# Performance work log

Measured on AMD Instinct MI355X. Metric: run time of the kernel, lower is better.

The kernel has to match this reference:

```python
import jax, jax.numpy as jnp
import numpy as np

N_BLOCK = 3; EMBED = 256; N_HEAD = 8; HEAD = EMBED // N_HEAD
N_AGENT = 8; SEQ = 256; BATCH = 64; ACT_DIM = 32
DECAY_SCALE = 1.0
EPS = 1e-6


def _decay_matrix():
    # Per-head decay kappas as in Mava Sable, decay over timesteps (pos // n_agent), causal mask.
    gammas = (1.0 - jnp.exp(jnp.linspace(jnp.log(1.0 / 32.0), jnp.log(1.0 / 512.0), N_HEAD))) * DECAY_SCALE
    t = (jnp.arange(SEQ) // N_AGENT).astype(jnp.float32)
    diff = t[:, None] - t[None, :]
    causal = jnp.arange(SEQ)[:, None] >= jnp.arange(SEQ)[None, :]
    return jnp.where(causal[None], gammas[:, None, None] ** diff[None], 0.0)  # [H,S,S]


def rmsnorm(x, scale):
    return x * jax.lax.rsqrt(jnp.mean(x * x, -1, keepdims=True) + EPS) * scale


def groupnorm(x, scale, bias):
    # GroupNorm with n_head groups over the feature dim, per position.
    B, S, E = x.shape
    xg = x.reshape(B, S, N_HEAD, HEAD)
    mu = xg.mean(-1, keepdims=True)
    var = ((xg - mu) ** 2).mean(-1, keepdims=True)
    xn = ((xg - mu) * jax.lax.rsqrt(var + 1e-5)).reshape(B, S, E)
    return xn * scale + bias


def retention(q_in, k_in, v_in, wq, wk, wv, wg, wo, gns, gnb, decay):
    # Parallel multi-scale retention: (Q K^T * D) V, groupnorm, swish gate from query input.
    B, S, E = q_in.shape
    q = (q_in @ wq).reshape(B, S, N_HEAD, HEAD).transpose(0, 2, 1, 3)
    k = (k_in @ wk).reshape(B, S, N_HEAD, HEAD).transpose(0, 2, 1, 3) / jnp.sqrt(jnp.float32(HEAD))
    v = (v_in @ wv).reshape(B, S, N_HEAD, HEAD).transpose(0, 2, 1, 3)
    scores = jnp.einsum('bhnd,bhmd->bhnm', q, k) * decay[None]
    ret = jnp.einsum('bhnm,bhmd->bhnd', scores, v)
    ret = groupnorm(ret.transpose(0, 2, 1, 3).reshape(B, S, E), gns, gnb)
    return (jax.nn.swish(q_in @ wg) * ret) @ wo


def swiglu(x, wg, w1, w2):
    return (jax.nn.swish(x @ wg) * (x @ w1)) @ w2


def forward(action, obs_rep, w_enc, ln0, wq1, wk1, wv1, wg1, wo1, gns1, gnb1, ln1,
            wq2, wk2, wv2, wg2, wo2, gns2, gnb2, ln2, swg, sw1, sw2, ln3,
            hw1, hb1, hln, hw2, hb2):
    decay = _decay_matrix()
    x = rmsnorm(jax.nn.gelu(action @ w_enc), ln0)
    for b in range(N_BLOCK):
        r1 = retention(x, x, x, wq1[b], wk1[b], wv1[b], wg1[b], wo1[b], gns1[b], gnb1[b], decay)
        x = rmsnorm(x + r1, ln1[b])
        r2 = retention(obs_rep, x, x, wq2[b], wk2[b], wv2[b], wg2[b], wo2[b], gns2[b], gnb2[b], decay)
        x = rmsnorm(obs_rep + r2, ln2[b])
        x = rmsnorm(x + swiglu(x, swg[b], sw1[b], sw2[b]), ln3[b])
    h = rmsnorm(jax.nn.gelu(x @ hw1 + hb1), hln)
    return h @ hw2 + hb2


def setup_inputs() -> dict:
    key = jax.random.key(0)
    ks = jax.random.split(key, 24)
    E, A, NB = EMBED, ACT_DIM, N_BLOCK
    s = 0.02
    return {
        'action': jax.random.uniform(ks[0], (BATCH, SEQ, A), jnp.float32),
        'obs_rep': jax.random.normal(ks[1], (BATCH, SEQ, E), jnp.float32),
        'w_enc': jax.random.normal(ks[2], (A, E), jnp.float32) * s,
        'ln0': jnp.ones((E,), jnp.float32),
        'wq1': jax.random.normal(ks[3], (NB, E, E), jnp.float32) * s,
        'wk1': jax.random.normal(ks[4], (NB, E, E), jnp.float32) * s,
        'wv1': jax.random.normal(ks[5], (NB, E, E), jnp.float32) * s,
        'wg1': jax.random.normal(ks[6], (NB, E, E), jnp.float32) * s,
        'wo1': jax.random.normal(ks[7], (NB, E, E), jnp.float32) * s,
        'gns1': jnp.ones((NB, E), jnp.float32),
        'gnb1': jnp.zeros((NB, E), jnp.float32),
        'ln1': jnp.ones((NB, E), jnp.float32),
        'wq2': jax.random.normal(ks[8], (NB, E, E), jnp.float32) * s,
        'wk2': jax.random.normal(ks[9], (NB, E, E), jnp.float32) * s,
        'wv2': jax.random.normal(ks[10], (NB, E, E), jnp.float32) * s,
        'wg2': jax.random.normal(ks[11], (NB, E, E), jnp.float32) * s,
        'wo2': jax.random.normal(ks[12], (NB, E, E), jnp.float32) * s,
        'gns2': jnp.ones((NB, E), jnp.float32),
        'gnb2': jnp.zeros((NB, E), jnp.float32),
        'ln2': jnp.ones((NB, E), jnp.float32),
        'swg': jax.random.normal(ks[13], (NB, E, E), jnp.float32) * s,
        'sw1': jax.random.normal(ks[14], (NB, E, E), jnp.float32) * s,
        'sw2': jax.random.normal(ks[15], (NB, E, E), jnp.float32) * s,
        'ln3': jnp.ones((NB, E), jnp.float32),
        'hw1': jax.random.normal(ks[16], (E, E), jnp.float32) * s,
        'hb1': jnp.zeros((E,), jnp.float32),
        'hln': jnp.ones((E,), jnp.float32),
        'hw2': jax.random.normal(ks[17], (E, A), jnp.float32) * s,
        'hb2': jnp.zeros((A,), jnp.float32),
    }


def reference(action, obs_rep, w_enc, ln0, wq1, wk1, wv1, wg1, wo1, gns1, gnb1, ln1,
              wq2, wk2, wv2, wg2, wo2, gns2, gnb2, ln2, swg, sw1, sw2, ln3,
              hw1, hb1, hln, hw2, hb2):
    return forward(action, obs_rep, w_enc, ln0, wq1, wk1, wv1, wg1, wo1, gns1, gnb1, ln1,
                   wq2, wk2, wv2, wg2, wo2, gns2, gnb2, ln2, swg, sw1, sw2, ln3,
                   hw1, hb1, hln, hw2, hb2)
```

## Files before the change

kernel.cpp:

```cpp
#include <hip/hip_runtime.h>
#include <cstdint>
#include <cmath>

typedef __attribute__((ext_vector_type(8))) short short8;
typedef __attribute__((ext_vector_type(4))) float floatx4;

#define DEV static __device__ __forceinline__

DEV float bf2f(uint16_t u) {
    union { uint32_t i; float f; } v; v.i = ((uint32_t)u) << 16; return v.f;
}
DEV uint16_t f2bf(float f) {
    union { float f; uint32_t i; } v; v.f = f;
    uint32_t r = (v.i + 0x7FFFu + ((v.i >> 16) & 1u)) >> 16;
    return (uint16_t)r;
}
DEV float swishf(float x) { return x / (1.f + __expf(-x)); }
DEV float geluf(float x) {
    const float c = 0.7978845608028654f;
    float t = tanhf(c * (x + 0.044715f * x * x * x));
    return 0.5f * x * (1.f + t);
}

#define CHUNK_E 8192
#define MAT_E   65536
#define APAD    264


struct TArg { const float* src[15]; };

__global__ __launch_bounds__(256) void tpose_k(TArg ta, uint16_t* __restrict__ arena) {
    int z = blockIdx.z;
    const float* src; uint16_t* dst;
    if (z == 0) {
        if (blockIdx.y) return;
        src = ta.src[0]; dst = arena;
    } else if (z <= 39) {
        int q = z - 1; int ti = q / 3, s = q % 3;
        src = ta.src[1 + ti] + (size_t)s * 65536;
        dst = arena + CHUNK_E + (size_t)(ti * 3 + s) * MAT_E;
    } else {
        src = ta.src[14]; dst = arena + CHUNK_E + (size_t)39 * MAT_E;
    }
    int k0 = blockIdx.y << 5;
    int n0 = blockIdx.x << 6;
    __shared__ __align__(16) uint16_t tile[32][72];
    int t = threadIdx.x;
    {
        int r = t >> 3, c = (t & 7) << 3;
        const float* s0 = src + (size_t)(k0 + r) * 256 + n0 + c;
        float4 f0 = *(const float4*)s0;
        float4 f1 = *(const float4*)(s0 + 4);
        tile[r][c + 0] = f2bf(f0.x); tile[r][c + 1] = f2bf(f0.y);
        tile[r][c + 2] = f2bf(f0.z); tile[r][c + 3] = f2bf(f0.w);
        tile[r][c + 4] = f2bf(f1.x); tile[r][c + 5] = f2bf(f1.y);
        tile[r][c + 6] = f2bf(f1.z); tile[r][c + 7] = f2bf(f1.w);
    }
    __syncthreads();
    {
        int n = t >> 2, c = (t & 3) << 3;
        uint16_t tmp[8];
#pragma unroll
        for (int j = 0; j < 8; ++j) tmp[j] = tile[c + j][n];
        *(uint4*)&dst[(size_t)(k0 >> 5) * CHUNK_E + (size_t)(n0 + n) * 32 + c] = *(uint4*)tmp;
    }
}

struct SegArgs {
    const float* action; const float* obs;
    uint16_t *actb, *obsb, *xb, *bq, *bk, *bv, *bg, *brg;
    const float *ln0, *hb1, *hln, *hw2, *hb2;
    float* outp;
    float l2g[8];
};

enum { EP2_NONE = 0, EP2_SWIGLU = 1 };

DEV void stage32(const uint16_t* __restrict__ g, int m0, uint16_t* __restrict__ lds) {
    const int t = threadIdx.x;
#pragma unroll
    for (int j = 0; j < 2; ++j) {
        int u = t + (j << 9);
        int r = u >> 5, cc = (u & 31) << 3;
        *(short8*)(lds + (size_t)r * APAD + cc) =
            *(const short8*)(g + (size_t)(m0 + r) * 256 + cc);
    }
}

template<bool AL, bool OG, bool RL, bool GELU>
DEV void gemm_ks(int m0, const uint16_t* __restrict__ A, const uint16_t* __restrict__ Wt,
                 uint16_t* __restrict__ Og, uint16_t* __restrict__ Ol,
                 const float* __restrict__ bias,
                 const uint16_t* __restrict__ Rg, const uint16_t* __restrict__ Rl,
                 const float* __restrict__ lnw,
                 float (&rowsum)[8][32], float (&red)[4][32][64])
{
    const int t = threadIdx.x;
    const int w = t >> 6, lane = t & 63, l16 = lane & 15, lg = lane >> 4;
    const int wc = w & 3, cb = wc << 6;
    const int kbase = (w >> 2) << 2;

    floatx4 acc[2][4];
#pragma unroll
    for (int i = 0; i < 2; ++i)
#pragma unroll
        for (int j = 0; j < 4; ++j) acc[i][j] = (floatx4){0.f, 0.f, 0.f, 0.f};

#pragma unroll
    for (int k2 = 0; k2 < 4; ++k2) {
        const int kc = kbase + k2;
        short8 aF[2], bF[4];
#pragma unroll
        for (int rt = 0; rt < 2; ++rt) {
            int row = (rt << 4) + l16;
            if constexpr (AL)
                aF[rt] = *(const short8*)(A + (size_t)row * APAD + (kc << 5) + (lg << 3));
            else
                aF[rt] = *(const short8*)(A + (size_t)(m0 + row) * 256 + (kc << 5) + (lg << 3));
        }
#pragma unroll
        for (int ct = 0; ct < 4; ++ct)
            bF[ct] = *(const short8*)(Wt + (size_t)kc * CHUNK_E +
                                      (size_t)(cb + (ct << 4) + l16) * 32 + (lg << 3));
#pragma unroll
        for (int rt = 0; rt < 2; ++rt)
#pragma unroll
            for (int ct = 0; ct < 4; ++ct)
                acc[rt][ct] = __builtin_amdgcn_mfma_f32_16x16x32_bf16(
                    aF[rt], bF[ct], acc[rt][ct], 0, 0, 0);
    }

    if (w >= 4) {
#pragma unroll
        for (int rt = 0; rt < 2; ++rt)
#pragma unroll
            for (int ct = 0; ct < 4; ++ct)
#pragma unroll
                for (int r = 0; r < 4; ++r)
                    red[wc][(rt << 4) | (ct << 2) | r][lane] = acc[rt][ct][r];
    }
    __syncthreads();

    float v[2][4][4];
    if (w < 4) {
#pragma unroll
        for (int rt = 0; rt < 2; ++rt)
#pragma unroll
            for (int ct = 0; ct < 4; ++ct)
#pragma unroll
                for (int r = 0; r < 4; ++r) {
                    int row = (rt << 4) + (lg << 2) + r;
                    int col = cb + (ct << 4) + l16;
                    float x = acc[rt][ct][r] + red[wc][(rt << 4) | (ct << 2) | r][lane];
                    if constexpr (GELU) {
                        if (bias) x += bias[col];
                        x = geluf(x);
                    } else {
                        if constexpr (RL) x += bf2f(Rl[(size_t)row * APAD + col]);
                        else              x += bf2f(Rg[(size_t)(m0 + row) * 256 + col]);
                    }
                    v[rt][ct][r] = x;
                }
#pragma unroll
        for (int rt = 0; rt < 2; ++rt)
#pragma unroll
            for (int r = 0; r < 4; ++r) {
                float p = 0.f;
#pragma unroll
                for (int ct = 0; ct < 4; ++ct) p += v[rt][ct][r] * v[rt][ct][r];
                p += __shfl_xor(p, 1, 64); p += __shfl_xor(p, 2, 64);
                p += __shfl_xor(p, 4, 64); p += __shfl_xor(p, 8, 64);
                int row = (rt << 4) + (lg << 2) + r;
                if (l16 == 0) rowsum[w][row] = p;
            }
    }
    __syncthreads();
    if (w < 4) {
#pragma unroll
        for (int rt = 0; rt < 2; ++rt)
#pragma unroll
            for (int r = 0; r < 4; ++r) {
                int row = (rt << 4) + (lg << 2) + r;
                float tot = rowsum[0][row] + rowsum[1][row] + rowsum[2][row] + rowsum[3][row];
                float rn = rsqrtf(tot * (1.f / 256.f) + 1e-6f);
#pragma unroll
                for (int ct = 0; ct < 4; ++ct) {
                    int col = cb + (ct << 4) + l16;
                    uint16_t bb = f2bf(v[rt][ct][r] * rn * lnw[col]);
                    if constexpr (OG)
                        Og[(size_t)(m0 + row) * 256 + col] = bb;
                    Ol[(size_t)row * APAD + col] = bb;
                }
            }
    }
    __syncthreads();
}

template<int EPI, bool AL>
DEV void gemm2_ws(int m0, const uint16_t* __restrict__ A,
                  const uint16_t* __restrict__ W1, const uint16_t* __restrict__ W2,
                  uint16_t* __restrict__ O1, uint16_t* __restrict__ O2,
                  uint16_t* __restrict__ Ol, float (&red)[4][32][64])
{
    const int t = threadIdx.x;
    const int w = t >> 6, lane = t & 63, l16 = lane & 15, lg = lane >> 4;
    const int wc = w & 3, cb = wc << 6;
    const uint16_t* W = (w < 4) ? W1 : W2;

    floatx4 acc[2][4];
#pragma unroll
    for (int i = 0; i < 2; ++i)
#pragma unroll
        for (int j = 0; j < 4; ++j) acc[i][j] = (floatx4){0.f, 0.f, 0.f, 0.f};

#pragma unroll
    for (int kc = 0; kc < 8; ++kc) {
        short8 aF[2], bF[4];
#pragma unroll
        for (int rt = 0; rt < 2; ++rt) {
            int row = (rt << 4) + l16;
            if constexpr (AL)
                aF[rt] = *(const short8*)(A + (size_t)row * APAD + (kc << 5) + (lg << 3));
            else
                aF[rt] = *(const short8*)(A + (size_t)(m0 + row) * 256 + (kc << 5) + (lg << 3));
        }
#pragma unroll
        for (int ct = 0; ct < 4; ++ct)
            bF[ct] = *(const short8*)(W + (size_t)kc * CHUNK_E +
                                      (size_t)(cb + (ct << 4) + l16) * 32 + (lg << 3));
#pragma unroll
        for (int rt = 0; rt < 2; ++rt)
#pragma unroll
            for (int ct = 0; ct < 4; ++ct)
                acc[rt][ct] = __builtin_amdgcn_mfma_f32_16x16x32_bf16(
                    aF[rt], bF[ct], acc[rt][ct], 0, 0, 0);
    }

    if constexpr (EPI == EP2_NONE) {
        uint16_t* O = (w < 4) ? O1 : O2;
#pragma unroll
        for (int rt = 0; rt < 2; ++rt)
#pragma unroll
            for (int ct = 0; ct < 4; ++ct)
#pragma unroll
                for (int r = 0; r < 4; ++r) {
                    int row = (rt << 4) + (lg << 2) + r;
                    int col = cb + (ct << 4) + l16;
                    O[(size_t)(m0 + row) * 256 + col] = f2bf(acc[rt][ct][r]);
                }
    } else {
        if (w >= 4) {
#pragma unroll
            for (int rt = 0; rt < 2; ++rt)
#pragma unroll
                for (int ct = 0; ct < 4; ++ct)
#pragma unroll
                    for (int r = 0; r < 4; ++r)
                        red[wc][(rt << 4) | (ct << 2) | r][lane] = acc[rt][ct][r];
        }
        __syncthreads();
        if (w < 4) {
#pragma unroll
            for (int rt = 0; rt < 2; ++rt)
#pragma unroll
                for (int ct = 0; ct < 4; ++ct)
#pragma unroll
                    for (int r = 0; r < 4; ++r) {
                        int row = (rt << 4) + (lg << 2) + r;
                        int col = cb + (ct << 4) + l16;
                        float up = red[wc][(rt << 4) | (ct << 2) | r][lane];
                        Ol[(size_t)row * APAD + col] = f2bf(swishf(acc[rt][ct][r]) * up);
                    }
        }
    }
}

DEV void gemm_enc(int m0, const uint16_t* __restrict__ A, const uint16_t* __restrict__ Wt,
                  uint16_t* __restrict__ Og, uint16_t* __restrict__ Ol,
                  const float* __restrict__ lnw, float (&rowsum)[8][32])
{
    const int t = threadIdx.x;
    const int w = t >> 6, lane = t & 63, l16 = lane & 15, lg = lane >> 4;

    floatx4 acc[2][2];
#pragma unroll
    for (int i = 0; i < 2; ++i)
#pragma unroll
        for (int j = 0; j < 2; ++j) acc[i][j] = (floatx4){0.f, 0.f, 0.f, 0.f};

    short8 aF[2], bF[2];
#pragma unroll
    for (int rt = 0; rt < 2; ++rt)
        aF[rt] = *(const short8*)(A + (size_t)((rt << 4) + l16) * 40 + (lg << 3));
#pragma unroll
    for (int ct = 0; ct < 2; ++ct)
        bF[ct] = *(const short8*)(Wt + (size_t)((w << 5) + (ct << 4) + l16) * 32 + (lg << 3));
#pragma unroll
    for (int rt = 0; rt < 2; ++rt)
#pragma unroll
        for (int ct = 0; ct < 2; ++ct)
            acc[rt][ct] = __builtin_amdgcn_mfma_f32_16x16x32_bf16(
                aF[rt], bF[ct], acc[rt][ct], 0, 0, 0);

    float v[2][2][4];
#pragma unroll
    for (int rt = 0; rt < 2; ++rt)
#pragma unroll
        for (int ct = 0; ct < 2; ++ct)
#pragma unroll
            for (int r = 0; r < 4; ++r)
                v[rt][ct][r] = geluf(acc[rt][ct][r]);

#pragma unroll
    for (int rt = 0; rt < 2; ++rt)
#pragma unroll
        for (int r = 0; r < 4; ++r) {
            float p = v[rt][0][r] * v[rt][0][r] + v[rt][1][r] * v[rt][1][r];
            p += __shfl_xor(p, 1, 64); p += __shfl_xor(p, 2, 64);
            p += __shfl_xor(p, 4, 64); p += __shfl_xor(p, 8, 64);
            int row = (rt << 4) + (lg << 2) + r;
            if (l16 == 0) rowsum[w][row] = p;
        }
    __syncthreads();
#pragma unroll
    for (int rt = 0; rt < 2; ++rt)
#pragma unroll
        for (int r = 0; r < 4; ++r) {
            int row = (rt << 4) + (lg << 2) + r;
            float tot = rowsum[0][row] + rowsum[1][row] + rowsum[2][row] + rowsum[3][row]
                      + rowsum[4][row] + rowsum[5][row] + rowsum[6][row] + rowsum[7][row];
            float rn = rsqrtf(tot * (1.f / 256.f) + 1e-6f);
#pragma unroll
            for (int ct = 0; ct < 2; ++ct) {
                int col = (w << 5) + (ct << 4) + l16;
                uint16_t bb = f2bf(v[rt][ct][r] * rn * lnw[col]);
                Og[(size_t)(m0 + row) * 256 + col] = bb;
                Ol[(size_t)row * APAD + col] = bb;
            }
        }
    __syncthreads();
}

DEV int rowbase(int blk) { return (blk & 63) * 256 + (blk >> 6) * 32; }


__global__ __launch_bounds__(512, 4) void seg0_k(SegArgs sa, const uint16_t* __restrict__ wenc,
                                                 const uint16_t* __restrict__ wq,
                                                 const uint16_t* __restrict__ wk,
                                                 const uint16_t* __restrict__ wv,
                                                 const uint16_t* __restrict__ wg)
{
    __shared__ float rowsum[8][32];
    __shared__ float red[4][32][64];
    __shared__ __align__(16) uint16_t actS[32][40];
    __shared__ __align__(16) uint16_t T0[32][APAD];
    const int t = threadIdx.x;
    const int m0 = rowbase(blockIdx.x);
    if (t < 256) {
        int r = t >> 3, c = (t & 7) << 2;
        float4 f = *(const float4*)(sa.action + (size_t)(m0 + r) * 32 + c);
        uint16_t tmp[4] = { f2bf(f.x), f2bf(f.y), f2bf(f.z), f2bf(f.w) };
        *(uint2*)&actS[r][c] = *(uint2*)tmp;
    }
    {
        const float4* ob = (const float4*)sa.obs + (size_t)m0 * 64;
        uint2* od = (uint2*)sa.obsb + (size_t)m0 * 64;
#pragma unroll
        for (int j = 0; j < 4; ++j) {
            float4 f = ob[(j << 9) + t];
            uint16_t tmp[4] = { f2bf(f.x), f2bf(f.y), f2bf(f.z), f2bf(f.w) };
            od[(j << 9) + t] = *(uint2*)tmp;
        }
    }
    __syncthreads();
    gemm_enc(m0, &actS[0][0], wenc, sa.xb, &T0[0][0], sa.ln0, rowsum);
    gemm2_ws<EP2_NONE, true>(m0, &T0[0][0], wq, wk, sa.bq, sa.bk, nullptr, red);
    gemm2_ws<EP2_NONE, true>(m0, &T0[0][0], wv, wg, sa.bv, sa.bg, nullptr, red);
}

__global__ __launch_bounds__(512, 4) void attn_k(SegArgs sa, const float* __restrict__ gns,
                                                 const float* __restrict__ gnb)
{
    __shared__ __align__(16) uint16_t QS[256][40];
    __shared__ __align__(16) uint16_t Ks[256][40];
    __shared__ __align__(16) uint16_t Vt[32][264];
    const int b = blockIdx.x & 63, h = blockIdx.x >> 6;
    const float l2g = sa.l2g[h];
    const int t = threadIdx.x, w = t >> 6, lane = t & 63, l16 = lane & 15, lg = lane >> 4;
    const size_t base = ((size_t)b * 256) * 256 + (size_t)h * 32;
    const uint16_t *q = sa.bq, *kbuf = sa.bk, *vbuf = sa.bv, *g = sa.bg;
    uint16_t* out = sa.brg;

    if (t < 256) {
        const uint4* qr = (const uint4*)(q + base + (size_t)t * 256);
        *(uint4*)&QS[t][0] = qr[0]; *(uint4*)&QS[t][8] = qr[1];
        *(uint4*)&QS[t][16] = qr[2]; *(uint4*)&QS[t][24] = qr[3];
        const uint4* kr = (const uint4*)(kbuf + base + (size_t)t * 256);
        *(uint4*)&Ks[t][0] = kr[0]; *(uint4*)&Ks[t][8] = kr[1];
        *(uint4*)&Ks[t][16] = kr[2]; *(uint4*)&Ks[t][24] = kr[3];
    } else {
        int c = t - 256;
        union { uint4 v4[4]; uint16_t u[32]; } vv;
        const uint4* vr = (const uint4*)(vbuf + base + (size_t)c * 256);
        vv.v4[0] = vr[0]; vv.v4[1] = vr[1]; vv.v4[2] = vr[2]; vv.v4[3] = vr[3];
#pragma unroll
        for (int d = 0; d < 32; ++d) Vt[d][c] = vv.u[d];
    }
    __syncthreads();

    const int iA = w, iB = 15 - w;
    short8 qFA = *(const short8*)&QS[(iA << 4) + l16][lg << 3];
    short8 qFB = *(const short8*)&QS[(iB << 4) + l16][lg << 3];

    const float invsq = 0.17677669529663687f;

    floatx4 raccA[2], raccB[2];
    raccA[0] = (floatx4){0,0,0,0}; raccA[1] = (floatx4){0,0,0,0};
    raccB[0] = (floatx4){0,0,0,0}; raccB[1] = (floatx4){0,0,0,0};

    auto do_strip = [&](int si, short8 qF, floatx4 (&racc)[2]) {
        const int jtmax = ((si << 4) + 15) >> 5;
        for (int jt = 0; jt <= jtmax; ++jt) {
            const int j0 = jt << 5;
            floatx4 sacc[2];
            sacc[0] = (floatx4){0,0,0,0}; sacc[1] = (floatx4){0,0,0,0};
            short8 kF[2];
#pragma unroll
            for (int ct = 0; ct < 2; ++ct)
                kF[ct] = *(const short8*)&Ks[j0 + (ct << 4) + l16][lg << 3];
#pragma unroll
            for (int ct = 0; ct < 2; ++ct)
                sacc[ct] = __builtin_amdgcn_mfma_f32_16x16x32_bf16(
                    qF, kF[ct], sacc[ct], 0, 0, 0);
#pragma unroll
            for (int ct = 0; ct < 2; ++ct)
#pragma unroll
                for (int r = 0; r < 4; ++r) {
                    int row16 = (lg << 2) + r;
                    int i = (si << 4) + row16;
                    int j = j0 + (ct << 4) + l16;
                    float svv = 0.f;
                    if (i >= j)
                        svv = sacc[ct][r] * invsq *
                              exp2f((float)((i >> 3) - (j >> 3)) * l2g);
                    QS[(si << 4) + row16][(ct << 4) + l16] = f2bf(svv);
                }
            short8 vF[2];
#pragma unroll
            for (int ct = 0; ct < 2; ++ct)
                vF[ct] = *(const short8*)&Vt[(ct << 4) + l16][j0 + (lg << 3)];
            short8 sF = *(const short8*)&QS[(si << 4) + l16][lg << 3];
#pragma unroll
            for (int ct = 0; ct < 2; ++ct)
                racc[ct] = __builtin_amdgcn_mfma_f32_16x16x32_bf16(
                    sF, vF[ct], racc[ct], 0, 0, 0);
        }
    };
    do_strip(iA, qFA, raccA);
    do_strip(iB, qFB, raccB);

    auto epi = [&](int si, floatx4 (&racc)[2]) {
#pragma unroll
        for (int r = 0; r < 4; ++r) {
            float v0 = racc[0][r], v1 = racc[1][r];
            float s1 = v0 + v1, s2 = v0 * v0 + v1 * v1;
            s1 += __shfl_xor(s1, 1, 64); s2 += __shfl_xor(s2, 1, 64);
            s1 += __shfl_xor(s1, 2, 64); s2 += __shfl_xor(s2, 2, 64);
            s1 += __shfl_xor(s1, 4, 64); s2 += __shfl_xor(s2, 4, 64);
            s1 += __shfl_xor(s1, 8, 64); s2 += __shfl_xor(s2, 8, 64);
            float mu = s1 * (1.f / 32.f);
            float var = s2 * (1.f / 32.f) - mu * mu;
            float rstd = rsqrtf(var + 1e-5f);
            int srow = (si << 4) + (lg << 2) + r;
            size_t obase = ((size_t)b * 256 + srow) * 256 + (size_t)h * 32;
#pragma unroll
            for (int ct = 0; ct < 2; ++ct) {
                int d = (ct << 4) + l16;
                float x = ct ? v1 : v0;
                float y = (x - mu) * rstd * gns[h * 32 + d] + gnb[h * 32 + d];
                float gv = swishf(bf2f(g[obase + d]));
                out[obase + d] = f2bf(y * gv);
            }
        }
    };
    epi(iA, raccA);
    epi(iB, raccB);
}

__global__ __launch_bounds__(512, 4) void g1_k(SegArgs sa,
    const uint16_t* __restrict__ wo, const float* __restrict__ ln1,
    const uint16_t* __restrict__ wq, const uint16_t* __restrict__ wk,
    const uint16_t* __restrict__ wv, const uint16_t* __restrict__ wg)
{
    __shared__ float rowsum[8][32];
    __shared__ float red[4][32][64];
    __shared__ __align__(16) uint16_t T0[32][APAD];
    __shared__ __align__(16) uint16_t T1[32][APAD];
    const int m0 = rowbase(blockIdx.x);
    stage32(sa.brg, m0, &T1[0][0]);
    __syncthreads();
    gemm_ks<true, false, false, false>(m0, &T1[0][0], wo,
        nullptr, &T0[0][0], nullptr, sa.xb, nullptr, ln1, rowsum, red);
    stage32(sa.obsb, m0, &T1[0][0]);
    gemm2_ws<EP2_NONE, true>(m0, &T0[0][0], wk, wv, sa.bk, sa.bv, nullptr, red);
    __syncthreads();
    gemm2_ws<EP2_NONE, true>(m0, &T1[0][0], wq, wg, sa.bq, sa.bg, nullptr, red);
}

__global__ __launch_bounds__(512, 4) void g2_k(SegArgs sa,
    const uint16_t* __restrict__ wo, const float* __restrict__ ln2,
    const uint16_t* __restrict__ wswg, const uint16_t* __restrict__ wsw1,
    const uint16_t* __restrict__ wsw2, const float* __restrict__ ln3,
    const uint16_t* __restrict__ nwq, const uint16_t* __restrict__ nwk,
    const uint16_t* __restrict__ nwv, const uint16_t* __restrict__ nwg)
{
    __shared__ float rowsum[8][32];
    __shared__ float red[4][32][64];
    __shared__ __align__(16) uint16_t T0[32][APAD];
    __shared__ __align__(16) uint16_t T1[32][APAD];
    const int m0 = rowbase(blockIdx.x);
    stage32(sa.brg, m0, &T1[0][0]);
    __syncthreads();
    gemm_ks<true, false, false, false>(m0, &T1[0][0], wo,
        nullptr, &T0[0][0], nullptr, sa.obsb, nullptr, ln2, rowsum, red);
    gemm2_ws<EP2_SWIGLU, true>(m0, &T0[0][0], wswg, wsw1, nullptr, nullptr, &T1[0][0], red);
    __syncthreads();
    gemm_ks<true, true, true, false>(m0, &T1[0][0], wsw2,
        sa.xb, &T0[0][0], nullptr, nullptr, &T0[0][0], ln3, rowsum, red);
    if (nwq) {
        gemm2_ws<EP2_NONE, true>(m0, &T0[0][0], nwq, nwk, sa.bq, sa.bk, nullptr, red);
        gemm2_ws<EP2_NONE, true>(m0, &T0[0][0], nwv, nwg, sa.bv, sa.bg, nullptr, red);
    }
}

__global__ __launch_bounds__(512, 4) void head_k(SegArgs sa, const uint16_t* __restrict__ hw1t)
{
    __shared__ float rowsum[8][32];
    __shared__ float red[4][32][64];
    __shared__ __align__(16) uint16_t T0[32][APAD];
    const int t = threadIdx.x;
    const int m0 = rowbase(blockIdx.x);
    gemm_ks<false, false, false, true>(m0, sa.xb, hw1t,
        nullptr, &T0[0][0], sa.hb1, nullptr, nullptr, sa.hln, rowsum, red);
    float* w2s = &red[0][0][0];
#pragma unroll
    for (int j = 0; j < 16; ++j) w2s[(j << 9) + t] = sa.hw2[(j << 9) + t];
    __syncthreads();
    {
        int n = t & 31, rs = t >> 5;
#pragma unroll
        for (int rr = 0; rr < 2; ++rr) {
            int lrow = (rr << 4) + rs;
            float a0 = sa.hb2[n];
#pragma unroll 8
            for (int kk = 0; kk < 256; ++kk)
                a0 += bf2f(T0[lrow][kk]) * w2s[kk * 32 + n];
            sa.outp[(size_t)(m0 + lrow) * 32 + n] = a0;
        }
    }
}

extern "C" void kernel_launch(void* const* d_in, const int* in_sizes, int n_in,
                              void* d_out, int out_size, void* d_ws, size_t ws_size,
                              hipStream_t stream)
{
    const float* action = (const float*)d_in[0];
    const float* obs    = (const float*)d_in[1];
    const float* w_enc  = (const float*)d_in[2];
    const float* ln0    = (const float*)d_in[3];
    const float* wq1 = (const float*)d_in[4];
    const float* wk1 = (const float*)d_in[5];
    const float* wv1 = (const float*)d_in[6];
    const float* wg1 = (const float*)d_in[7];
    const float* wo1 = (const float*)d_in[8];
    const float* gns1 = (const float*)d_in[9];
    const float* gnb1 = (const float*)d_in[10];
    const float* ln1  = (const float*)d_in[11];
    const float* wq2 = (const float*)d_in[12];
    const float* wk2 = (const float*)d_in[13];
    const float* wv2 = (const float*)d_in[14];
    const float* wg2 = (const float*)d_in[15];
    const float* wo2 = (const float*)d_in[16];
    const float* gns2 = (const float*)d_in[17];
    const float* gnb2 = (const float*)d_in[18];
    const float* ln2  = (const float*)d_in[19];
    const float* swgp = (const float*)d_in[20];
    const float* sw1p = (const float*)d_in[21];
    const float* sw2p = (const float*)d_in[22];
    const float* ln3  = (const float*)d_in[23];
    const float* hw1  = (const float*)d_in[24];
    const float* hb1  = (const float*)d_in[25];
    const float* hln  = (const float*)d_in[26];
    const float* hw2  = (const float*)d_in[27];
    const float* hb2  = (const float*)d_in[28];

    char* ws = (char*)d_ws;
    uint16_t* wt   = (uint16_t*)(ws + 0);
    uint16_t* actb = (uint16_t*)(ws + 6291456);
    uint16_t* obsb = (uint16_t*)(ws + 7340032);
    uint16_t* xb   = (uint16_t*)(ws + 15728640);
    uint16_t* bq   = (uint16_t*)(ws + 24117248);
    uint16_t* bk   = (uint16_t*)(ws + 32505856);
    uint16_t* bv   = (uint16_t*)(ws + 40894464);
    uint16_t* bg   = (uint16_t*)(ws + 49283072);
    uint16_t* brg  = (uint16_t*)(ws + 57671680);

    uint16_t* wtenc = wt;
    uint16_t* hw1t  = wt + CHUNK_E + (size_t)39 * MAT_E;
    auto WTp = [&](int ti, int s) { return wt + CHUNK_E + (size_t)(ti * 3 + s) * MAT_E; };

    TArg ta;
    ta.src[0] = w_enc;
    ta.src[1] = wq1;  ta.src[2] = wk1;  ta.src[3] = wv1;  ta.src[4] = wg1;  ta.src[5] = wo1;
    ta.src[6] = wq2;  ta.src[7] = wk2;  ta.src[8] = wv2;  ta.src[9] = wg2;  ta.src[10] = wo2;
    ta.src[11] = swgp; ta.src[12] = sw1p; ta.src[13] = sw2p; ta.src[14] = hw1;
    tpose_k<<<dim3(4, 8, 41), 256, 0, stream>>>(ta, wt);

    SegArgs sa;
    sa.action = action; sa.obs = obs;
    sa.actb = actb; sa.obsb = obsb; sa.xb = xb;
    sa.bq = bq; sa.bk = bk; sa.bv = bv; sa.bg = bg; sa.brg = brg;
    sa.ln0 = ln0; sa.hb1 = hb1; sa.hln = hln; sa.hw2 = hw2; sa.hb2 = hb2;
    sa.outp = (float*)d_out;
    {
        const double a = log(1.0 / 32.0), bb = log(1.0 / 512.0);
        for (int hh = 0; hh < 8; ++hh) {
            double lg = a + (bb - a) * hh / 7.0;
            double gam = 1.0 - exp(lg);
            sa.l2g[hh] = (float)(log(gam) / log(2.0));
        }
    }

    dim3 GB(512), TB(512);
    seg0_k<<<GB, TB, 0, stream>>>(sa, wtenc, WTp(0, 0), WTp(1, 0), WTp(2, 0), WTp(3, 0));
    for (int b3 = 0; b3 < 3; ++b3) {
        attn_k<<<GB, TB, 0, stream>>>(sa, gns1 + b3 * 256, gnb1 + b3 * 256);
        g1_k<<<GB, TB, 0, stream>>>(sa, WTp(4, b3), ln1 + b3 * 256,
                                    WTp(5, b3), WTp(6, b3), WTp(7, b3), WTp(8, b3));
        attn_k<<<GB, TB, 0, stream>>>(sa, gns2 + b3 * 256, gnb2 + b3 * 256);
        g2_k<<<GB, TB, 0, stream>>>(sa, WTp(9, b3), ln2 + b3 * 256,
                                    WTp(10, b3), WTp(11, b3), WTp(12, b3), ln3 + b3 * 256,
                                    b3 < 2 ? WTp(0, b3 + 1) : nullptr,
                                    b3 < 2 ? WTp(1, b3 + 1) : nullptr,
                                    b3 < 2 ? WTp(2, b3 + 1) : nullptr,
                                    b3 < 2 ? WTp(3, b3 + 1) : nullptr);
    }
    head_k<<<GB, TB, 0, stream>>>(sa, hw1t);
}
```

Measured before the change: 496.1 us.

## Prefetch weight fragments up front and split split-K epilogue across all waves

In the split-K GEMM, all weight fragments for a wave's K half are loaded into registers before the MFMA loop. The reduction is restructured so each K-half wave group finishes one row tile, which spreads the residual/GELU, RMSNorm and store epilogue over all 8 waves instead of 4. In the two-weight GEMM, weight fragments are loaded in a double-buffered prefetch so the second half's loads overlap the first half's MFMAs. The aim is to hide global weight-load latency and remove idle waves in the epilogue, at the cost of more registers (16 short8 fragments per wave), which may reduce occupancy or cause spills.

```diff
diff --git a/kernel.cpp b/kernel.cpp
--- a/kernel.cpp
+++ b/kernel.cpp
@@ -98,7 +98,16 @@
     const int t = threadIdx.x;
     const int w = t >> 6, lane = t & 63, l16 = lane & 15, lg = lane >> 4;
     const int wc = w & 3, cb = wc << 6;
-    const int kbase = (w >> 2) << 2;
+    const int kh = w >> 2;
+    const int kbase = kh << 2;
+
+    short8 bF[4][4];
+#pragma unroll
+    for (int k2 = 0; k2 < 4; ++k2)
+#pragma unroll
+        for (int ct = 0; ct < 4; ++ct)
+            bF[k2][ct] = *(const short8*)(Wt + (size_t)(kbase + k2) * CHUNK_E +
+                                          (size_t)(cb + (ct << 4) + l16) * 32 + (lg << 3));
 
     floatx4 acc[2][4];
 #pragma unroll
@@ -109,7 +118,7 @@
 #pragma unroll
     for (int k2 = 0; k2 < 4; ++k2) {
         const int kc = kbase + k2;
-        short8 aF[2], bF[4];
+        short8 aF[2];
 #pragma unroll
         for (int rt = 0; rt < 2; ++rt) {
             int row = (rt << 4) + l16;
@@ -119,79 +128,85 @@
                 aF[rt] = *(const short8*)(A + (size_t)(m0 + row) * 256 + (kc << 5) + (lg << 3));
         }
 #pragma unroll
-        for (int ct = 0; ct < 4; ++ct)
-            bF[ct] = *(const short8*)(Wt + (size_t)kc * CHUNK_E +
-                                      (size_t)(cb + (ct << 4) + l16) * 32 + (lg << 3));
-#pragma unroll
         for (int rt = 0; rt < 2; ++rt)
 #pragma unroll
             for (int ct = 0; ct < 4; ++ct)
                 acc[rt][ct] = __builtin_amdgcn_mfma_f32_16x16x32_bf16(
-                    aF[rt], bF[ct], acc[rt][ct], 0, 0, 0);
-    }
-
-    if (w >= 4) {
-#pragma unroll
-        for (int rt = 0; rt < 2; ++rt)
-#pragma unroll
-            for (int ct = 0; ct < 4; ++ct)
-#pragma unroll
-                for (int r = 0; r < 4; ++r)
-                    red[wc][(rt << 4) | (ct << 2) | r][lane] = acc[rt][ct][r];
-    }
-    __syncthreads();
-
-    float v[2][4][4];
-    if (w < 4) {
-#pragma unroll
-        for (int rt = 0; rt < 2; ++rt)
-#pragma unroll
-            for (int ct = 0; ct < 4; ++ct)
-#pragma unroll
-                for (int r = 0; r < 4; ++r) {
-                    int row = (rt << 4) + (lg << 2) + r;
-                    int col = cb + (ct << 4) + l16;
-                    float x = acc[rt][ct][r] + red[wc][(rt << 4) | (ct << 2) | r][lane];
-                    if constexpr (GELU) {
-                        if (bias) x += bias[col];
-                        x = geluf(x);
-                    } else {
-                        if constexpr (RL) x += bf2f(Rl[(size_t)row * APAD + col]);
-                        else              x += bf2f(Rg[(size_t)(m0 + row) * 256 + col]);
-                    }
-                    v[rt][ct][r] = x;
-                }
-#pragma unroll
-        for (int rt = 0; rt < 2; ++rt)
-#pragma unroll
-            for (int r = 0; r < 4; ++r) {
-                float p = 0.f;
-#pragma unroll
-                for (int ct = 0; ct < 4; ++ct) p += v[rt][ct][r] * v[rt][ct][r];
-                p += __shfl_xor(p, 1, 64); p += __shfl_xor(p, 2, 64);
-                p += __shfl_xor(p, 4, 64); p += __shfl_xor(p, 8, 64);
-                int row = (rt << 4) + (lg << 2) + r;
-                if (l16 == 0) rowsum[w][row] = p;
+                    aF[rt], bF[k2][ct], acc[rt][ct], 0, 0, 0);
+    }
+
+    if (kh == 0) {
+#pragma unroll
+        for (int ct = 0; ct < 4; ++ct)
+#pragma unroll
+            for (int r = 0; r < 4; ++r)
+                red[wc][16 | (ct << 2) | r][lane] = acc[1][ct][r];
+    } else {
+#pragma unroll
+        for (int ct = 0; ct < 4; ++ct)
+#pragma unroll
+            for (int r = 0; r < 4; ++r)
+                red[wc][(ct << 2) | r][lane] = acc[0][ct][r];
+    }
+    __syncthreads();
+
+    float v[4][4];
+    if (kh == 0) {
+#pragma unroll
+        for (int ct = 0; ct < 4; ++ct)
+#pragma unroll
+            for (int r = 0; r < 4; ++r)
+                v[ct][r] = acc[0][ct][r] + red[wc][(ct << 2) | r][lane];
+    } else {
+#pragma unroll
+        for (int ct = 0; ct < 4; ++ct)
+#pragma unroll
+            for (int r = 0; r < 4; ++r)
+                v[ct][r] = acc[1][ct][r] + red[wc][16 | (ct << 2) | r][lane];
+    }
+
+    const int rbase = kh << 4;
+#pragma unroll
+    for (int ct = 0; ct < 4; ++ct)
+#pragma unroll
+        for (int r = 0; r < 4; ++r) {
+            int row = rbase + (lg << 2) + r;
+            int col = cb + (ct << 4) + l16;
+            float x = v[ct][r];
+            if constexpr (GELU) {
+                if (bias) x += bias[col];
+                x = geluf(x);
+            } else {
+                if constexpr (RL) x += bf2f(Rl[(size_t)row * APAD + col]);
+                else              x += bf2f(Rg[(size_t)(m0 + row) * 256 + col]);
             }
-    }
-    __syncthreads();
-    if (w < 4) {
-#pragma unroll
-        for (int rt = 0; rt < 2; ++rt)
-#pragma unroll
-            for (int r = 0; r < 4; ++r) {
-                int row = (rt << 4) + (lg << 2) + r;
-                float tot = rowsum[0][row] + rowsum[1][row] + rowsum[2][row] + rowsum[3][row];
-                float rn = rsqrtf(tot * (1.f / 256.f) + 1e-6f);
-#pragma unroll
-                for (int ct = 0; ct < 4; ++ct) {
-                    int col = cb + (ct << 4) + l16;
-                    uint16_t bb = f2bf(v[rt][ct][r] * rn * lnw[col]);
-                    if constexpr (OG)
-                        Og[(size_t)(m0 + row) * 256 + col] = bb;
-                    Ol[(size_t)row * APAD + col] = bb;
-                }
-            }
+            v[ct][r] = x;
+        }
+
+#pragma unroll
+    for (int r = 0; r < 4; ++r) {
+        float p = 0.f;
+#pragma unroll
+        for (int ct = 0; ct < 4; ++ct) p += v[ct][r] * v[ct][r];
+        p += __shfl_xor(p, 1, 64); p += __shfl_xor(p, 2, 64);
+        p += __shfl_xor(p, 4, 64); p += __shfl_xor(p, 8, 64);
+        int row = rbase + (lg << 2) + r;
+        if (l16 == 0) rowsum[wc][row] = p;
+    }
+    __syncthreads();
+#pragma unroll
+    for (int r = 0; r < 4; ++r) {
+        int row = rbase + (lg << 2) + r;
+        float tot = rowsum[0][row] + rowsum[1][row] + rowsum[2][row] + rowsum[3][row];
+        float rn = rsqrtf(tot * (1.f / 256.f) + 1e-6f);
+#pragma unroll
+        for (int ct = 0; ct < 4; ++ct) {
+            int col = cb + (ct << 4) + l16;
+            uint16_t bb = f2bf(v[ct][r] * rn * lnw[col]);
+            if constexpr (OG)
+                Og[(size_t)(m0 + row) * 256 + col] = bb;
+            Ol[(size_t)row * APAD + col] = bb;
+        }
     }
     __syncthreads();
 }
@@ -206,6 +221,7 @@
     const int w = t >> 6, lane = t & 63, l16 = lane & 15, lg = lane >> 4;
     const int wc = w & 3, cb = wc << 6;
     const uint16_t* W = (w < 4) ? W1 : W2;
+    const size_t wcol = (size_t)(cb + l16) * 32 + (lg << 3);
 
     floatx4 acc[2][4];
 #pragma unroll
@@ -213,9 +229,40 @@
 #pragma unroll
         for (int j = 0; j < 4; ++j) acc[i][j] = (floatx4){0.f, 0.f, 0.f, 0.f};
 
-#pragma unroll
-    for (int kc = 0; kc < 8; ++kc) {
-        short8 aF[2], bF[4];
+    short8 bF[4][4];
+#pragma unroll
+    for (int k2 = 0; k2 < 4; ++k2)
+#pragma unroll
+        for (int ct = 0; ct < 4; ++ct)
+            bF[k2][ct] = *(const short8*)(W + (size_t)k2 * CHUNK_E + wcol +
+                                          (size_t)(ct << 4) * 32);
+
+#pragma unroll
+    for (int k2 = 0; k2 < 4; ++k2) {
+        short8 aF[2];
+#pragma unroll
+        for (int rt = 0; rt < 2; ++rt) {
+            int row = (rt << 4) + l16;
+            if constexpr (AL)
+                aF[rt] = *(const short8*)(A + (size_t)row * APAD + (k2 << 5) + (lg << 3));
+            else
+                aF[rt] = *(const short8*)(A + (size_t)(m0 + row) * 256 + (k2 << 5) + (lg << 3));
+        }
+#pragma unroll
+        for (int rt = 0; rt < 2; ++rt)
+#pragma unroll
+            for (int ct = 0; ct < 4; ++ct)
+                acc[rt][ct] = __builtin_amdgcn_mfma_f32_16x16x32_bf16(
+                    aF[rt], bF[k2][ct], acc[rt][ct], 0, 0, 0);
+#pragma unroll
+        for (int ct = 0; ct < 4; ++ct)
+            bF[k2][ct] = *(const short8*)(W + (size_t)(k2 + 4) * CHUNK_E + wcol +
+                                          (size_t)(ct << 4) * 32);
+    }
+#pragma unroll
+    for (int k2 = 0; k2 < 4; ++k2) {
+        const int kc = k2 + 4;
+        short8 aF[2];
 #pragma unroll
         for (int rt = 0; rt < 2; ++rt) {
             int row = (rt << 4) + l16;
@@ -225,15 +272,11 @@
                 aF[rt] = *(const short8*)(A + (size_t)(m0 + row) * 256 + (kc << 5) + (lg << 3));
         }
 #pragma unroll
-        for (int ct = 0; ct < 4; ++ct)
-            bF[ct] = *(const short8*)(W + (size_t)kc * CHUNK_E +
-                                      (size_t)(cb + (ct << 4) + l16) * 32 + (lg << 3));
-#pragma unroll
         for (int rt = 0; rt < 2; ++rt)
 #pragma unroll
             for (int ct = 0; ct < 4; ++ct)
                 acc[rt][ct] = __builtin_amdgcn_mfma_f32_16x16x32_bf16(
-                    aF[rt], bF[ct], acc[rt][ct], 0, 0, 0);
+                    aF[rt], bF[k2][ct], acc[rt][ct], 0, 0, 0);
     }
 
     if constexpr (EPI == EP2_NONE) {
```

Result: slower. 507.1 us (+2.2%).
